# Kernel optimization log

Hardware: AMD Instinct MI355X
Metric: run time of the kernel (lower is better)

Reference implementation:

```python
import jax, jax.numpy as jnp
import numpy as np

NUM_HEADS = 12
DIM_HEAD = 64
HIDDEN = 768


def _get_rel_pos(size, rel_pos):
    # q_size == k_size: relative coords in [0, 2*size-2]
    idx = jnp.arange(size)[:, None] - jnp.arange(size)[None, :] + (size - 1)
    return rel_pos[idx]  # (size, size, dim_head)


def setup_inputs() -> dict:
    key = jax.random.key(0)
    ks = jax.random.split(key, 5)
    B, H, W, C = 4, 32, 32, HIDDEN
    x = jax.random.normal(ks[0], (B, H, W, C), dtype=jnp.float32)
    w_qkv = jax.random.normal(ks[1], (C, 3 * NUM_HEADS * DIM_HEAD), dtype=jnp.float32) * (C ** -0.5)
    w_out = jax.random.normal(ks[2], (NUM_HEADS * DIM_HEAD, C), dtype=jnp.float32) * ((NUM_HEADS * DIM_HEAD) ** -0.5)
    b_out = jnp.zeros((C,), dtype=jnp.float32)
    rel_pos_h = jax.random.normal(ks[3], (2 * H - 1, DIM_HEAD), dtype=jnp.float32) * 0.02
    rel_pos_w = jax.random.normal(ks[4], (2 * W - 1, DIM_HEAD), dtype=jnp.float32) * 0.02
    return {"x": x, "w_qkv": w_qkv, "w_out": w_out, "b_out": b_out,
            "rel_pos_h": rel_pos_h, "rel_pos_w": rel_pos_w}


def reference(x, w_qkv, w_out, b_out, rel_pos_h, rel_pos_w):
    B, H, W, C = x.shape
    N = H * W
    nh, dh = NUM_HEADS, DIM_HEAD
    # qkv projection: (B, N, 3*nh*dh) split as (qkv, head, dim)
    qkv = x.reshape(B, N, C) @ w_qkv
    qkv = qkv.reshape(B, N, 3, nh, dh).transpose(2, 0, 3, 1, 4)  # (3, B, nh, N, dh)
    q, k, v = qkv[0], qkv[1], qkv[2]
    scale = dh ** -0.5
    attn = jnp.einsum('bhnd,bhmd->bhnm', q, k) * scale  # (B, nh, N, N)
    # decomposed relative positional bias (heads folded into batch)
    Rh = _get_rel_pos(H, rel_pos_h)  # (H, H, dh)
    Rw = _get_rel_pos(W, rel_pos_w)  # (W, W, dh)
    r_q = q.reshape(B * nh, H, W, dh)
    rel_h = jnp.einsum('bhwc,hkc->bhwk', r_q, Rh)  # (B*nh, H, W, H)
    rel_w = jnp.einsum('bhwc,wkc->bhwk', r_q, Rw)  # (B*nh, H, W, W)
    attn = (attn.reshape(B * nh, H, W, H, W)
            + rel_h[:, :, :, :, None]
            + rel_w[:, :, :, None, :]).reshape(B, nh, N, N)
    attn = jax.nn.softmax(attn, axis=-1)
    out = jnp.einsum('bhnm,bhmd->bhnd', attn, v)  # (B, nh, N, dh)
    out = out.transpose(0, 2, 1, 3).reshape(B, N, nh * dh)
    return out @ w_out + b_out  # (B, N, hidden)
```

## Files before the change

### kernel.cpp

```cpp
#include <hip/hip_runtime.h>
#include <cstdint>

#define DEV __device__ __forceinline__

typedef __bf16  bf16x8 __attribute__((ext_vector_type(8)));
typedef short   s16x8  __attribute__((ext_vector_type(8)));
typedef float   f32x4  __attribute__((ext_vector_type(4)));

#define QSCALE 0.18033688011112042f
#define MOFF   17.312340490667560f

DEV unsigned short f2bf(float f){
  union { float f; unsigned u; } v; v.f = f;
  unsigned r = v.u + 0x7fffu + ((v.u >> 16) & 1u);
  return (unsigned short)(r >> 16);
}

DEV unsigned pk2(float lo, float hi){
  unsigned a = __builtin_bit_cast(unsigned, lo) + 0x8000u;
  unsigned b = __builtin_bit_cast(unsigned, hi) + 0x8000u;
  return __builtin_amdgcn_perm(b, a, 0x07060302);
}

DEV void gl2lds16(const void* g, void* l){
  __builtin_amdgcn_global_load_lds((__attribute__((address_space(1))) void*)(void*)(g),
                                   (__attribute__((address_space(3))) void*)(l), 16, 0, 0);
}

DEV f32x4 mfma16(bf16x8 a, bf16x8 b, f32x4 c){
  return __builtin_amdgcn_mfma_f32_16x16x32_bf16(a, b, c, 0, 0, 0);
}

__global__ __launch_bounds__(256) void prep_kernel(const float* __restrict__ x,
                                                   short* __restrict__ xb,
                                                   const float* __restrict__ rph,
                                                   const float* __restrict__ rpw,
                                                   short* __restrict__ rphb,
                                                   short* __restrict__ rpwb,
                                                   const float* __restrict__ w_qkv,
                                                   short* __restrict__ wqT,
                                                   const float* __restrict__ w_out,
                                                   short* __restrict__ woT){
  __shared__ float tb[32][33];
  int b = blockIdx.x;
  if (b < 1536){
    int i = b * 256 + threadIdx.x;
    const float4* in4 = (const float4*)x;
    float4 f0 = in4[i*2], f1 = in4[i*2+1];
    s16x8 o;
    o[0]=(short)f2bf(f0.x); o[1]=(short)f2bf(f0.y); o[2]=(short)f2bf(f0.z); o[3]=(short)f2bf(f0.w);
    o[4]=(short)f2bf(f1.x); o[5]=(short)f2bf(f1.y); o[6]=(short)f2bf(f1.z); o[7]=(short)f2bf(f1.w);
    *(s16x8*)(xb + i*8) = o;
  } else if (b == 1536){
    int t = threadIdx.x;
    for (int j = 0; j < 16; j++){
      int idx = t*16 + j;
      if (idx < 4032){
        rphb[idx] = (short)f2bf(rph[idx] * 8.f);
        rpwb[idx] = (short)f2bf(rpw[idx] * 8.f);
      }
    }
  } else {
    const float* in; short* out; int R, C, bx, by;
    if (b < 3265){ int t = b - 1537; in = w_qkv; out = wqT; R = 768; C = 2304; bx = t % 72; by = t / 72; }
    else         { int t = b - 3265; in = w_out; out = woT; R = 768; C = 768;  bx = t % 24; by = t / 24; }
    int tx = threadIdx.x & 31, ty = threadIdx.x >> 5;
    int c0 = bx * 32, r0 = by * 32;
    for (int i = 0; i < 4; i++)
      tb[ty + i*8][tx] = in[(r0 + ty + i*8)*C + c0 + tx];
    __syncthreads();
    for (int i = 0; i < 4; i++)
      out[(c0 + ty + i*8)*R + r0 + tx] = (short)f2bf(tb[tx][ty + i*8]);
  }
}

__global__ __launch_bounds__(256) void qkv_gemm_kernel(const short* __restrict__ xb,
                                                       const short* __restrict__ wqT,
                                                       short* __restrict__ qb,
                                                       short* __restrict__ kb,
                                                       short* __restrict__ vb){
  __shared__ __align__(16) short As[128*64];
  __shared__ __align__(16) short Bs[128*64];
  const int tid = threadIdx.x, lane = tid & 63, wv = tid >> 6;
  const int quad = lane >> 4, mi = lane & 15;
  const int m0 = blockIdx.x * 128, n0 = blockIdx.y * 128;
  const int wrow = wv >> 1, wcol = wv & 1;
  const int srow = lane >> 3, scs = lane & 7;
  const int sc = scs ^ (srow & 7);
  f32x4 acc[4][4] = {};
  for (int k0 = 0; k0 < 768; k0 += 64){
    __syncthreads();
    for (int i = 0; i < 4; i++){
      int rbase = i*32 + wv*8;
      int row = rbase + srow;
      gl2lds16(xb  + (m0+row)*768 + k0 + sc*8, As + rbase*64 + lane*8);
      gl2lds16(wqT + (n0+row)*768 + k0 + sc*8, Bs + rbase*64 + lane*8);
    }
    __syncthreads();
    bf16x8 a[2][4], b[2][4];
#pragma unroll
    for (int kk = 0; kk < 2; kk++){
      int ccs = ((quad + kk*4) ^ (mi & 7)) * 8;
      for (int mt = 0; mt < 4; mt++) a[kk][mt] = *(const bf16x8*)(As + (wrow*64 + mt*16 + mi)*64 + ccs);
      for (int nt = 0; nt < 4; nt++) b[kk][nt] = *(const bf16x8*)(Bs + (wcol*64 + nt*16 + mi)*64 + ccs);
    }
#pragma unroll
    for (int kk = 0; kk < 2; kk++)
      for (int mt = 0; mt < 4; mt++)
        for (int nt = 0; nt < 4; nt++)
          acc[mt][nt] = mfma16(a[kk][mt], b[kk][nt], acc[mt][nt]);
  }
  const int which = n0 / 768;
  const float qs = (which == 0) ? QSCALE : 1.0f;
  for (int nt = 0; nt < 4; nt++){
    int j = n0 + wcol*64 + nt*16 + mi;
    int rem = j % 768;
    int head = rem >> 6, d = rem & 63;
    short* dst = (which == 0) ? qb : (which == 1) ? kb : vb;
    for (int mt = 0; mt < 4; mt++)
      for (int r = 0; r < 4; r++){
        int m = m0 + wrow*64 + mt*16 + quad*4 + r;
        int bh = (m >> 10)*12 + head;
        dst[((bh << 10) + (m & 1023))*64 + d] = (short)f2bf(acc[mt][nt][r] * qs);
      }
  }
}

__global__ __launch_bounds__(256) void relvt_kernel(const short* __restrict__ qb,
                                                    const short* __restrict__ rphb,
                                                    const short* __restrict__ rpwb,
                                                    float* __restrict__ relHT,
                                                    float* __restrict__ relW,
                                                    const short* __restrict__ vb,
                                                    short* __restrict__ vtb){
  __shared__ __align__(16) short T[64*64];
  if (blockIdx.x < 1536){
    int wv = threadIdx.x >> 6, lane = threadIdx.x & 63;
    int bid = blockIdx.x*4 + wv;
    int quad = lane >> 4, mi = lane & 15;
    f32x4 acc[2] = {};
    if (bid < 3072){
      int bh = bid >> 6, rest = bid & 63, h = rest >> 1, half = rest & 1;
      const short* qr = qb + (bh*1024 + h*32 + half*16 + mi)*64;
      bf16x8 a0 = *(const bf16x8*)(qr + quad*8);
      bf16x8 a1 = *(const bf16x8*)(qr + 32 + quad*8);
      for (int nt = 0; nt < 2; nt++){
        int kh = nt*16 + mi;
        const short* rr = rphb + (h - kh + 31)*64;
        bf16x8 b0 = *(const bf16x8*)(rr + quad*8);
        bf16x8 b1 = *(const bf16x8*)(rr + 32 + quad*8);
        acc[nt] = mfma16(a0, b0, acc[nt]);
        acc[nt] = mfma16(a1, b1, acc[nt]);
      }
      for (int nt = 0; nt < 2; nt++){
        f32x4 o;
        for (int r = 0; r < 4; r++) o[r] = acc[nt][r] - MOFF;
        *(f32x4*)&relHT[bh*32768 + (nt*16 + mi)*1024 + h*32 + half*16 + quad*4] = o;
      }
    } else {
      int bid2 = bid - 3072, w = bid2 / 96, rt = bid2 % 96;
      int rg = rt*16 + mi, bh = rg >> 5, h = rg & 31;
      const short* qr = qb + (bh*1024 + h*32 + w)*64;
      bf16x8 a0 = *(const bf16x8*)(qr + quad*8);
      bf16x8 a1 = *(const bf16x8*)(qr + 32 + quad*8);
      for (int nt = 0; nt < 2; nt++){
        int kw = nt*16 + mi;
        const short* rr = rpwb + (w - kw + 31)*64;
        bf16x8 b0 = *(const bf16x8*)(rr + quad*8);
        bf16x8 b1 = *(const bf16x8*)(rr + 32 + quad*8);
        acc[nt] = mfma16(a0, b0, acc[nt]);
        acc[nt] = mfma16(a1, b1, acc[nt]);
      }
      for (int nt = 0; nt < 2; nt++)
        for (int r = 0; r < 4; r++){
          int rowg = rt*16 + quad*4 + r;
          relW[(rowg*32 + w)*32 + nt*16 + mi] = acc[nt][r];
        }
    }
  } else {
    int blk = blockIdx.x - 1536;
    int t = threadIdx.x;
    int bh = blk >> 4, t0 = (blk & 15) * 64;
    const short* src = vb + (bh*1024 + t0)*64;
    for (int p = 0; p < 2; p++){
      int row = p*32 + (t >> 3);
      int c = (t & 7) ^ (row & 7);
      gl2lds16(src + row*64 + c*8, T + p*2048 + t*8);
    }
    __syncthreads();
    int d = t >> 2, k4 = t & 3;
    short vals[16];
    for (int j = 0; j < 16; j++){
      int k = k4 + j*4;
      int cs = (d >> 3) ^ (k & 7);
      vals[j] = T[k*64 + cs*8 + (d & 7)];
    }
    short* dst = vtb + (bh*64 + d)*1024 + t0;
    for (int j = 0; j < 16; j++)
      dst[k4 + j*4] = vals[j];
  }
}

__global__ __launch_bounds__(256, 3) void flash_kernel(const short* __restrict__ qb,
                                                       const short* __restrict__ kb,
                                                       const short* __restrict__ vtb,
                                                       const float* __restrict__ relHT,
                                                       const float* __restrict__ relW,
                                                       short* __restrict__ ao){
  __shared__ __align__(16) short Qt[64*64];
  __shared__ __align__(16) short Kt[64*64];
  __shared__ __align__(16) short Vt[64*64];
  __shared__ __align__(16) short Pt[64*64];
  __shared__ __align__(16) float rHs[32*64];
  __shared__ __align__(16) float rWs[64*32];
  const int tid = threadIdx.x, lane = tid & 63, wv = tid >> 6;
  const int quad = lane >> 4, mi = lane & 15;
  const int bh = blockIdx.y, n0 = blockIdx.x * 64;
  const int sw0 = (quad ^ (mi & 7)) * 8;
  const int sw1 = ((quad + 4) ^ (mi & 7)) * 8;
  const int qrow = wv*16 + mi;
  const int srow = lane >> 3;

  const short* kg = kb  + bh*1024*64;
  const short* vg = vtb + bh*64*1024;

  {
    const short* qg  = qb    + (bh*1024 + n0)*64;
    const float* rhg = relHT + bh*32768 + n0;
    const float* rwg = relW  + (bh*1024 + n0)*32;
    for (int i = 0; i < 2; i++){
      int slab = wv*2 + i, rbase = slab*8;
      int row = rbase + srow;
      int c = (lane & 7) ^ (row & 7);
      gl2lds16(qg + row*64 + c*8, Qt + rbase*64 + lane*8);
      int khrow = i*16 + wv*4 + (lane >> 4);
      gl2lds16(rhg + khrow*1024 + (lane & 15)*4, rHs + i*1024 + wv*256 + lane*4);
      gl2lds16(rwg + slab*256 + lane*4, rWs + slab*256 + lane*4);
    }
  }
  __syncthreads();

  bf16x8 qf0 = *(const bf16x8*)(Qt + qrow*64 + sw0);
  bf16x8 qf1 = *(const bf16x8*)(Qt + qrow*64 + sw1);
  float rw[2][4];
#pragma unroll
  for (int s = 0; s < 2; s++)
    for (int r = 0; r < 4; r++)
      rw[s][r] = rWs[qrow*32 + s*16 + quad*4 + r];

  f32x4 O[4] = {};
  float l_ = 0.f;

  for (int step = 0; step < 16; step++){
    {
      const short* kt = kg + step*64*64;
      for (int i = 0; i < 2; i++){
        int slab = wv*2 + i, rbase = slab*8;
        int row = rbase + srow;
        int c = (lane & 7) ^ (row & 7);
        gl2lds16(kt + row*64 + c*8, Kt + rbase*64 + lane*8);
        gl2lds16(vg + row*1024 + step*64 + c*8, Vt + rbase*64 + lane*8);
      }
    }
    __syncthreads();

    f32x4 S[4];
#pragma unroll
    for (int nt = 0; nt < 4; nt++){
      bf16x8 kf0 = *(const bf16x8*)(Kt + (nt*16 + mi)*64 + sw0);
      bf16x8 kf1 = *(const bf16x8*)(Kt + (nt*16 + mi)*64 + sw1);
      f32x4 c = {};
      c = mfma16(kf0, qf0, c);
      c = mfma16(kf1, qf1, c);
      S[nt] = c;
    }
    float kh0 = rHs[(2*step)*64 + qrow];
    float kh1 = rHs[(2*step + 1)*64 + qrow];
#pragma unroll
    for (int nt = 0; nt < 4; nt++){
      float kh = (nt & 2) ? kh1 : kh0;
      for (int r = 0; r < 4; r++){
        float p = __builtin_amdgcn_exp2f(S[nt][r] + kh + rw[nt & 1][r]);
        S[nt][r] = p;
        l_ += p;
      }
    }
#pragma unroll
    for (int nt = 0; nt < 4; nt++){
      unsigned u0 = pk2(S[nt][0], S[nt][1]);
      unsigned u1 = pk2(S[nt][2], S[nt][3]);
      int chunk = (2*nt + (quad >> 1)) ^ (mi & 7);
      uint2 uu; uu.x = u0; uu.y = u1;
      *(uint2*)(Pt + qrow*64 + chunk*8 + (quad & 1)*4) = uu;
    }
    bf16x8 p0 = *(const bf16x8*)(Pt + qrow*64 + sw0);
    bf16x8 p1 = *(const bf16x8*)(Pt + qrow*64 + sw1);
#pragma unroll
    for (int t = 0; t < 4; t++){
      bf16x8 v0 = *(const bf16x8*)(Vt + (t*16 + mi)*64 + sw0);
      bf16x8 v1 = *(const bf16x8*)(Vt + (t*16 + mi)*64 + sw1);
      O[t] = mfma16(p0, v0, O[t]);
      O[t] = mfma16(p1, v1, O[t]);
    }
    __syncthreads();
  }

  l_ += __shfl_xor(l_, 16, 64);
  l_ += __shfl_xor(l_, 32, 64);
  float inv[4];
#pragma unroll
  for (int r = 0; r < 4; r++) inv[r] = 1.f / __shfl(l_, quad*4 + r, 64);
  int b_ = bh / 12, head = bh % 12;
#pragma unroll
  for (int t = 0; t < 4; t++)
    for (int r = 0; r < 4; r++){
      int n = n0 + wv*16 + quad*4 + r;
      ao[(b_*1024 + n)*768 + head*64 + t*16 + mi] = (short)f2bf(O[t][r] * inv[r]);
    }
}

__global__ __launch_bounds__(256) void proj_kernel(const short* __restrict__ ao,
                                                   const short* __restrict__ woT,
                                                   const float* __restrict__ bias,
                                                   float* __restrict__ out){
  __shared__ __align__(16) short As[128*64];
  __shared__ __align__(16) short Bs[64*64];
  const int tid = threadIdx.x, lane = tid & 63, wv = tid >> 6;
  const int quad = lane >> 4, mi = lane & 15;
  const int m0 = blockIdx.x * 128, n0 = blockIdx.y * 64;
  const int srow = lane >> 3, sc = (lane & 7) ^ (srow & 7);
  f32x4 acc[2][4] = {};
  for (int k0 = 0; k0 < 768; k0 += 64){
    __syncthreads();
    for (int i = 0; i < 4; i++){
      int rbase = i*32 + wv*8, row = rbase + srow;
      gl2lds16(ao + (m0+row)*768 + k0 + sc*8, As + rbase*64 + lane*8);
    }
    for (int i = 0; i < 2; i++){
      int rbase = i*32 + wv*8, row = rbase + srow;
      gl2lds16(woT + (n0+row)*768 + k0 + sc*8, Bs + rbase*64 + lane*8);
    }
    __syncthreads();
#pragma unroll
    for (int kk = 0; kk < 2; kk++){
      int ccs = ((quad + kk*4) ^ (mi & 7)) * 8;
      bf16x8 a[2], b[4];
      for (int mt = 0; mt < 2; mt++) a[mt] = *(const bf16x8*)(As + (wv*32 + mt*16 + mi)*64 + ccs);
      for (int nt = 0; nt < 4; nt++) b[nt] = *(const bf16x8*)(Bs + (nt*16 + mi)*64 + ccs);
      for (int mt = 0; mt < 2; mt++)
        for (int nt = 0; nt < 4; nt++)
          acc[mt][nt] = mfma16(a[mt], b[nt], acc[mt][nt]);
    }
  }
  for (int nt = 0; nt < 4; nt++){
    int j = n0 + nt*16 + mi;
    float bj = bias[j];
    for (int mt = 0; mt < 2; mt++)
      for (int r = 0; r < 4; r++){
        int m = m0 + wv*32 + mt*16 + quad*4 + r;
        out[m*768 + j] = acc[mt][nt][r] + bj;
      }
  }
}

extern "C" void kernel_launch(void* const* d_in, const int* in_sizes, int n_in,
                              void* d_out, int out_size, void* d_ws, size_t ws_size,
                              hipStream_t stream){
  const float* x     = (const float*)d_in[0];
  const float* w_qkv = (const float*)d_in[1];
  const float* w_out = (const float*)d_in[2];
  const float* b_out = (const float*)d_in[3];
  const float* rph   = (const float*)d_in[4];
  const float* rpw   = (const float*)d_in[5];
  float* out = (float*)d_out;
  char* ws = (char*)d_ws;
  short* xb    = (short*)(ws + 0);
  short* wqT   = (short*)(ws + 6291456);
  short* woT   = (short*)(ws + 9830400);
  short* qb    = (short*)(ws + 11010048);
  short* kb    = (short*)(ws + 17301504);
  short* vb    = (short*)(ws + 23592960);
  short* vtb   = (short*)(ws + 29884416);
  float* relHT = (float*)(ws + 36175872);
  float* relW  = (float*)(ws + 42467328);
  short* rphb  = (short*)(ws + 48758784);
  short* rpwb  = (short*)(ws + 48775168);
  short* ao    = xb;

  prep_kernel<<<3841, 256, 0, stream>>>(x, xb, rph, rpw, rphb, rpwb, w_qkv, wqT, w_out, woT);
  qkv_gemm_kernel<<<dim3(32, 18), 256, 0, stream>>>(xb, wqT, qb, kb, vb);
  relvt_kernel<<<2304, 256, 0, stream>>>(qb, rphb, rpwb, relHT, relW, vb, vtb);
  flash_kernel<<<dim3(16, 48), 256, 0, stream>>>(qb, kb, vtb, relHT, relW, ao);
  proj_kernel<<<dim3(32, 12), 256, 0, stream>>>(ao, woT, b_out, out);
}
```

Baseline: 165.9 us.

## Process 128 query rows per flash block to reuse K/V tiles across two sub-tiles

Each flash-attention block now handles two 64-row query tiles, reusing every K and V tile staged in LDS for both and halving the grid to 8x48 blocks. This cuts global K/V traffic and barriers per query row. The P staging buffer now aliases the Q LDS region, since Q fragments sit in registers after the first barrier, and relW values are read straight from global into registers instead of through LDS. The cost is more registers per thread (two accumulator sets) and only 384 blocks, which may leave the GPU underfilled.

```diff
diff --git a/kernel.cpp b/kernel.cpp
--- a/kernel.cpp
+++ b/kernel.cpp
@@ -207,15 +207,13 @@
                                                        const float* __restrict__ relHT,
                                                        const float* __restrict__ relW,
                                                        short* __restrict__ ao){
-  __shared__ __align__(16) short Qt[64*64];
+  __shared__ __align__(16) short Qt[2*64*64];
   __shared__ __align__(16) short Kt[64*64];
   __shared__ __align__(16) short Vt[64*64];
-  __shared__ __align__(16) short Pt[64*64];
-  __shared__ __align__(16) float rHs[32*64];
-  __shared__ __align__(16) float rWs[64*32];
+  __shared__ __align__(16) float rHs[2*32*64];
   const int tid = threadIdx.x, lane = tid & 63, wv = tid >> 6;
   const int quad = lane >> 4, mi = lane & 15;
-  const int bh = blockIdx.y, n0 = blockIdx.x * 64;
+  const int bh = blockIdx.y, q0 = blockIdx.x * 128;
   const int sw0 = (quad ^ (mi & 7)) * 8;
   const int sw1 = ((quad + 4) ^ (mi & 7)) * 8;
   const int qrow = wv*16 + mi;
@@ -225,31 +223,36 @@
   const short* vg = vtb + bh*64*1024;
 
   {
-    const short* qg  = qb    + (bh*1024 + n0)*64;
-    const float* rhg = relHT + bh*32768 + n0;
-    const float* rwg = relW  + (bh*1024 + n0)*32;
-    for (int i = 0; i < 2; i++){
-      int slab = wv*2 + i, rbase = slab*8;
+    const short* qg  = qb + (bh*1024 + q0)*64;
+    const float* rhg = relHT + bh*32768 + q0;
+    for (int i = 0; i < 4; i++){
+      int slab = wv*4 + i, rbase = slab*8;
       int row = rbase + srow;
       int c = (lane & 7) ^ (row & 7);
       gl2lds16(qg + row*64 + c*8, Qt + rbase*64 + lane*8);
-      int khrow = i*16 + wv*4 + (lane >> 4);
-      gl2lds16(rhg + khrow*1024 + (lane & 15)*4, rHs + i*1024 + wv*256 + lane*4);
-      gl2lds16(rwg + slab*256 + lane*4, rWs + slab*256 + lane*4);
+      int tt = i >> 1, ii = i & 1;
+      int khrow = ii*16 + wv*4 + (lane >> 4);
+      gl2lds16(rhg + khrow*1024 + tt*64 + (lane & 15)*4,
+               rHs + tt*2048 + ii*1024 + wv*256 + lane*4);
     }
   }
   __syncthreads();
 
-  bf16x8 qf0 = *(const bf16x8*)(Qt + qrow*64 + sw0);
-  bf16x8 qf1 = *(const bf16x8*)(Qt + qrow*64 + sw1);
-  float rw[2][4];
-#pragma unroll
-  for (int s = 0; s < 2; s++)
-    for (int r = 0; r < 4; r++)
-      rw[s][r] = rWs[qrow*32 + s*16 + quad*4 + r];
-
-  f32x4 O[4] = {};
-  float l_ = 0.f;
+  bf16x8 qf0[2], qf1[2];
+  float rw[2][2][4];
+  float l_[2] = {0.f, 0.f};
+  f32x4 O[2][4] = {};
+#pragma unroll
+  for (int t = 0; t < 2; t++){
+    qf0[t] = *(const bf16x8*)(Qt + (t*64 + qrow)*64 + sw0);
+    qf1[t] = *(const bf16x8*)(Qt + (t*64 + qrow)*64 + sw1);
+    const float* rwg = relW + (bh*1024 + q0 + t*64 + qrow)*32;
+    for (int s = 0; s < 2; s++){
+      float4 v4 = *(const float4*)(rwg + s*16 + quad*4);
+      rw[t][s][0]=v4.x; rw[t][s][1]=v4.y; rw[t][s][2]=v4.z; rw[t][s][3]=v4.w;
+    }
+  }
+  short* Pt = Qt;
 
   for (int step = 0; step < 16; step++){
     {
@@ -264,59 +267,64 @@
     }
     __syncthreads();
 
-    f32x4 S[4];
-#pragma unroll
-    for (int nt = 0; nt < 4; nt++){
-      bf16x8 kf0 = *(const bf16x8*)(Kt + (nt*16 + mi)*64 + sw0);
-      bf16x8 kf1 = *(const bf16x8*)(Kt + (nt*16 + mi)*64 + sw1);
-      f32x4 c = {};
-      c = mfma16(kf0, qf0, c);
-      c = mfma16(kf1, qf1, c);
-      S[nt] = c;
-    }
-    float kh0 = rHs[(2*step)*64 + qrow];
-    float kh1 = rHs[(2*step + 1)*64 + qrow];
-#pragma unroll
-    for (int nt = 0; nt < 4; nt++){
-      float kh = (nt & 2) ? kh1 : kh0;
+#pragma unroll
+    for (int t = 0; t < 2; t++){
+      f32x4 S[4];
+#pragma unroll
+      for (int nt = 0; nt < 4; nt++){
+        bf16x8 kf0 = *(const bf16x8*)(Kt + (nt*16 + mi)*64 + sw0);
+        bf16x8 kf1 = *(const bf16x8*)(Kt + (nt*16 + mi)*64 + sw1);
+        f32x4 c = {};
+        c = mfma16(kf0, qf0[t], c);
+        c = mfma16(kf1, qf1[t], c);
+        S[nt] = c;
+      }
+      float kh0 = rHs[t*2048 + (2*step)*64 + qrow];
+      float kh1 = rHs[t*2048 + (2*step + 1)*64 + qrow];
+#pragma unroll
+      for (int nt = 0; nt < 4; nt++){
+        float kh = (nt & 2) ? kh1 : kh0;
+        for (int r = 0; r < 4; r++){
+          float p = __builtin_amdgcn_exp2f(S[nt][r] + kh + rw[t][nt & 1][r]);
+          S[nt][r] = p;
+          l_[t] += p;
+        }
+      }
+#pragma unroll
+      for (int nt = 0; nt < 4; nt++){
+        unsigned u0 = pk2(S[nt][0], S[nt][1]);
+        unsigned u1 = pk2(S[nt][2], S[nt][3]);
+        int chunk = (2*nt + (quad >> 1)) ^ (mi & 7);
+        uint2 uu; uu.x = u0; uu.y = u1;
+        *(uint2*)(Pt + qrow*64 + chunk*8 + (quad & 1)*4) = uu;
+      }
+      bf16x8 p0 = *(const bf16x8*)(Pt + qrow*64 + sw0);
+      bf16x8 p1 = *(const bf16x8*)(Pt + qrow*64 + sw1);
+#pragma unroll
+      for (int tt = 0; tt < 4; tt++){
+        bf16x8 v0 = *(const bf16x8*)(Vt + (tt*16 + mi)*64 + sw0);
+        bf16x8 v1 = *(const bf16x8*)(Vt + (tt*16 + mi)*64 + sw1);
+        O[t][tt] = mfma16(p0, v0, O[t][tt]);
+        O[t][tt] = mfma16(p1, v1, O[t][tt]);
+      }
+    }
+    __syncthreads();
+  }
+
+  int b_ = bh / 12, head = bh % 12;
+#pragma unroll
+  for (int t = 0; t < 2; t++){
+    float l = l_[t];
+    l += __shfl_xor(l, 16, 64);
+    l += __shfl_xor(l, 32, 64);
+    float inv[4];
+    for (int r = 0; r < 4; r++) inv[r] = 1.f / __shfl(l, quad*4 + r, 64);
+    for (int tt = 0; tt < 4; tt++)
       for (int r = 0; r < 4; r++){
-        float p = __builtin_amdgcn_exp2f(S[nt][r] + kh + rw[nt & 1][r]);
-        S[nt][r] = p;
-        l_ += p;
-      }
-    }
-#pragma unroll
-    for (int nt = 0; nt < 4; nt++){
-      unsigned u0 = pk2(S[nt][0], S[nt][1]);
-      unsigned u1 = pk2(S[nt][2], S[nt][3]);
-      int chunk = (2*nt + (quad >> 1)) ^ (mi & 7);
-      uint2 uu; uu.x = u0; uu.y = u1;
-      *(uint2*)(Pt + qrow*64 + chunk*8 + (quad & 1)*4) = uu;
-    }
-    bf16x8 p0 = *(const bf16x8*)(Pt + qrow*64 + sw0);
-    bf16x8 p1 = *(const bf16x8*)(Pt + qrow*64 + sw1);
-#pragma unroll
-    for (int t = 0; t < 4; t++){
-      bf16x8 v0 = *(const bf16x8*)(Vt + (t*16 + mi)*64 + sw0);
-      bf16x8 v1 = *(const bf16x8*)(Vt + (t*16 + mi)*64 + sw1);
-      O[t] = mfma16(p0, v0, O[t]);
-      O[t] = mfma16(p1, v1, O[t]);
-    }
-    __syncthreads();
-  }
-
-  l_ += __shfl_xor(l_, 16, 64);
-  l_ += __shfl_xor(l_, 32, 64);
-  float inv[4];
-#pragma unroll
-  for (int r = 0; r < 4; r++) inv[r] = 1.f / __shfl(l_, quad*4 + r, 64);
-  int b_ = bh / 12, head = bh % 12;
-#pragma unroll
-  for (int t = 0; t < 4; t++)
-    for (int r = 0; r < 4; r++){
-      int n = n0 + wv*16 + quad*4 + r;
-      ao[(b_*1024 + n)*768 + head*64 + t*16 + mi] = (short)f2bf(O[t][r] * inv[r]);
-    }
+        int n = q0 + t*64 + wv*16 + quad*4 + r;
+        ao[(b_*1024 + n)*768 + head*64 + tt*16 + mi] = (short)f2bf(O[t][tt][r] * inv[r]);
+      }
+  }
 }
 
 __global__ __launch_bounds__(256) void proj_kernel(const short* __restrict__ ao,
@@ -390,6 +398,6 @@
   prep_kernel<<<3841, 256, 0, stream>>>(x, xb, rph, rpw, rphb, rpwb, w_qkv, wqT, w_out, woT);
   qkv_gemm_kernel<<<dim3(32, 18), 256, 0, stream>>>(xb, wqT, qb, kb, vb);
   relvt_kernel<<<2304, 256, 0, stream>>>(qb, rphb, rpwb, relHT, relW, vb, vtb);
-  flash_kernel<<<dim3(16, 48), 256, 0, stream>>>(qb, kb, vtb, relHT, relW, ao);
+  flash_kernel<<<dim3(8, 48), 256, 0, stream>>>(qb, kb, vtb, relHT, relW, ao);
   proj_kernel<<<dim3(32, 12), 256, 0, stream>>>(ao, woT, b_out, out);
 }
```

Measured after the change: 179.1 us. 7.9% more time.
